# Optimization experiments

Measured on AMD Instinct MI355X. Metric: run time of the kernel, lower is better.

## Reference

```python
import jax, jax.numpy as jnp
import numpy as np

D = 128        # d_model
G = 2          # gnn_layers
LE = 2         # e_layers (MLP depth per update fn)
N_NODES = 20000
N_EDGES = 320000
SEQ = 72       # label_len(48) + pred_len(24)
DEC_IN = 4
PRED_LEN = 24
C_OUT = 1
EPS = 1e-5


def _ln(x, g, b):
    m = jnp.mean(x, axis=-1, keepdims=True)
    v = jnp.var(x, axis=-1, keepdims=True)
    return (x - m) * jax.lax.rsqrt(v + EPS) * g + b


def _mlp(x, ws, bs, gs, betas):
    # MLPLayer stack: LayerNorm(gelu(Linear(x))); dropout=0 in eval
    for i in range(ws.shape[0]):
        x = _ln(jax.nn.gelu(x @ ws[i] + bs[i]), gs[i], betas[i])
    return x


def setup_inputs():
    key = jax.random.key(0)
    ks = list(jax.random.split(key, 16))
    s = 0.02
    f32 = jnp.float32
    inp = {}
    inp["nodes"] = jax.random.normal(ks[0], (N_NODES, SEQ, DEC_IN), f32)
    inp["edges"] = jax.random.normal(ks[1], (N_EDGES, 2), f32)
    inp["senders"] = jax.random.randint(ks[2], (N_EDGES,), 0, N_NODES, jnp.int32)
    inp["receivers"] = jax.random.randint(ks[3], (N_EDGES,), 0, N_NODES, jnp.int32)
    inp["w_node_emb"] = jax.random.normal(ks[4], (SEQ * DEC_IN, D), f32) * s
    inp["b_node_emb"] = jnp.zeros((D,), f32)
    inp["w_edge_emb"] = jax.random.normal(ks[5], (2, D), f32) * s
    inp["b_edge_emb"] = jnp.zeros((D,), f32)
    inp["edge_proj_w"] = jax.random.normal(ks[6], (G, 3 * D, D), f32) * s
    inp["edge_proj_b"] = jnp.zeros((G, D), f32)
    inp["node_proj_w"] = jax.random.normal(ks[7], (G, 2 * D, D), f32) * s
    inp["node_proj_b"] = jnp.zeros((G, D), f32)
    inp["edge_mlp_w"] = jax.random.normal(ks[8], (G, LE, D, D), f32) * s
    inp["edge_mlp_b"] = jnp.zeros((G, LE, D), f32)
    inp["edge_ln_g"] = jnp.ones((G, LE, D), f32)
    inp["edge_ln_b"] = jnp.zeros((G, LE, D), f32)
    inp["node_mlp_w"] = jax.random.normal(ks[9], (G, LE, D, D), f32) * s
    inp["node_mlp_b"] = jnp.zeros((G, LE, D), f32)
    inp["node_ln_g"] = jnp.ones((G, LE, D), f32)
    inp["node_ln_b"] = jnp.zeros((G, LE, D), f32)
    inp["mlp_out_w"] = jax.random.normal(ks[10], (D, D), f32) * s
    inp["mlp_out_b"] = jnp.zeros((D,), f32)
    inp["mlp_out_g"] = jnp.ones((D,), f32)
    inp["mlp_out_beta"] = jnp.zeros((D,), f32)
    inp["proj_w"] = jax.random.normal(ks[11], (D, C_OUT * PRED_LEN), f32) * s
    inp["proj_b"] = jnp.zeros((C_OUT * PRED_LEN,), f32)
    return inp


def reference(nodes, edges, senders, receivers, w_node_emb, b_node_emb, w_edge_emb, b_edge_emb, edge_proj_w, edge_proj_b, node_proj_w, node_proj_b, edge_mlp_w, edge_mlp_b, edge_ln_g, edge_ln_b, node_mlp_w, node_mlp_b, node_ln_g, node_ln_b, mlp_out_w, mlp_out_b, mlp_out_g, mlp_out_beta, proj_w, proj_b):
    N = nodes.shape[0]
    # embeddings
    h = nodes.reshape(N, -1) @ w_node_emb + b_node_emb          # [N, D]
    e = edges @ w_edge_emb + b_edge_emb                         # [E, D]
    # receiver in-degree for unsorted_mean_agg (clamped to avoid /0)
    cnt = jax.ops.segment_sum(jnp.ones(e.shape[:1], h.dtype), receivers, num_segments=N)
    cnt = jnp.maximum(cnt, 1.0)[:, None]                        # [N, 1]
    for l in range(G):
        # edge update: gather endpoint node states, project to D, MLP, residual
        e_in = jnp.concatenate([e, h[senders], h[receivers]], axis=-1)   # [E, 3D]
        e = e + _mlp(e_in @ edge_proj_w[l] + edge_proj_b[l],
                     edge_mlp_w[l], edge_mlp_b[l], edge_ln_g[l], edge_ln_b[l])
        # scatter-mean aggregation of updated edges into receiver nodes
        agg = jax.ops.segment_sum(e, receivers, num_segments=N) / cnt    # [N, D]
        # node update
        n_in = jnp.concatenate([h, agg], axis=-1)                        # [N, 2D]
        h = h + _mlp(n_in @ node_proj_w[l] + node_proj_b[l],
                     node_mlp_w[l], node_mlp_b[l], node_ln_g[l], node_ln_b[l])
    # output MLP + projection to pred_len * c_out per node
    h = _ln(jax.nn.gelu(h @ mlp_out_w + mlp_out_b), mlp_out_g, mlp_out_beta)
    out = h @ proj_w + proj_b
    return out.reshape(N, PRED_LEN, C_OUT)
```

## Files before the change

kernel.cpp:

```cpp
#include <hip/hip_runtime.h>
#include <hip/hip_bf16.h>
#include <stdint.h>

typedef unsigned short ushort_t;
typedef __attribute__((ext_vector_type(8))) short short8;
typedef __attribute__((ext_vector_type(4))) short short4v;
typedef __attribute__((ext_vector_type(4))) float f32x4;
typedef __attribute__((ext_vector_type(4))) int int4v;

#define N_NODES 20000
#define N_EDGES 320000
#define D 128
#define XSTRIDE 136

#define GAS __attribute__((address_space(1)))
#define LAS __attribute__((address_space(3)))

__device__ __forceinline__ float b2f(ushort_t u) {
    union { float f; uint32_t i; } v; v.i = ((uint32_t)u) << 16; return v.f;
}
__device__ __forceinline__ ushort_t f2b(float f) {
    __bf16 h = (__bf16)f;
    return __builtin_bit_cast(ushort_t, h);
}
__device__ __forceinline__ float ldf(const void* p, size_t i, bool f32) {
    return f32 ? ((const float*)p)[i] : b2f(((const ushort_t*)p)[i]);
}
__device__ __forceinline__ short8 lda8(const void* p, size_t i, bool f32) {
    if (f32) {
        const float* fp = (const float*)p + i;
        f32x4 v0 = *(const f32x4*)fp;
        f32x4 v1 = *(const f32x4*)(fp + 4);
        short8 a;
#pragma unroll
        for (int j = 0; j < 4; ++j) {
            a[j]     = (short)f2b(v0[j]);
            a[j + 4] = (short)f2b(v1[j]);
        }
        return a;
    }
    return *(const short8*)((const ushort_t*)p + i);
}
__device__ __forceinline__ float gelu_tanh(float x) {
    float u = 0.7978845608028654f * (x + 0.044715f * x * x * x);
    u = fminf(fmaxf(u, -15.f), 15.f);
    float e = __expf(2.f * u);
    float t = (e - 1.f) * __builtin_amdgcn_rcpf(e + 1.f);
    return 0.5f * x * (1.f + t);
}
__device__ __forceinline__ int clampi(int v, int hi) {
    return v < 0 ? 0 : (v >= hi ? hi - 1 : v);
}
__device__ __forceinline__ void gload_lds16(const void* g, void* l) {
    __builtin_amdgcn_global_load_lds((const GAS uint32_t*)g, (LAS uint32_t*)l, 16, 0, 0);
}
__device__ __forceinline__ void ldedge(const void* edges, int row, bool f32, float& a0, float& a1) {
    if (f32) {
        const float* p = (const float*)edges + (size_t)row * 2;
        a0 = p[0]; a1 = p[1];
    } else {
        const ushort_t* p = (const ushort_t*)edges + (size_t)row * 2;
        a0 = b2f(p[0]); a1 = b2f(p[1]);
    }
}
__device__ __forceinline__ short8 einit8(const ushort_t* wedge, int colbase, float a0, float a1) {
    short8 w0 = *(const short8*)(wedge + colbase);
    short8 w1 = *(const short8*)(wedge + 128 + colbase);
    short8 bb = *(const short8*)(wedge + 256 + colbase);
    short8 r;
#pragma unroll
    for (int j = 0; j < 8; ++j)
        r[j] = (short)f2b(a0 * b2f((ushort_t)w0[j]) + a1 * b2f((ushort_t)w1[j]) + b2f((ushort_t)bb[j]));
    return r;
}

__device__ __forceinline__ void ln8(float x[8], const float gv[8], const float bv[8]) {
    float s1 = 0.f, s2 = 0.f;
#pragma unroll
    for (int n = 0; n < 8; ++n) { s1 += x[n]; s2 += x[n] * x[n]; }
#pragma unroll
    for (int m = 1; m < 16; m <<= 1) {
        s1 += __shfl_xor(s1, m, 64);
        s2 += __shfl_xor(s2, m, 64);
    }
    float mean = s1 * (1.f / 128.f);
    float var  = fmaxf(s2 * (1.f / 128.f) - mean * mean, 0.f);
    float rs   = __builtin_amdgcn_rsqf(var + 1e-5f);
#pragma unroll
    for (int n = 0; n < 8; ++n) x[n] = (x[n] - mean) * rs * gv[n] + bv[n];
}

__global__ void k_detect(const uint32_t* __restrict__ raw, int* __restrict__ flag) {
    int t = blockIdx.x * blockDim.x + threadIdx.x;
    uint32_t u = raw[t];
    int e_lo = (u >> 7)  & 0xFF;
    int e_hi = (u >> 23) & 0xFF;
    if (e_lo == 0xFF || e_hi == 0xFF) atomicOr(flag, 1);
}

struct SetupArgs {
    const void* psrc[15];
    int         pn[15];
    int         pdst[15];
    const void* fsrc[6];
    int         fkb[6];
    int         fdst[6];
    const void* projw;
};

__global__ void k_setup(SetupArgs a, ushort_t* __restrict__ bvec, ushort_t* __restrict__ frag,
                        ushort_t* __restrict__ wT, const int* __restrict__ dflag) {
    const bool f32 = *dflag != 0;
    int t = blockIdx.x * blockDim.x + threadIdx.x;
    if (t < 4608) {
        int i = t, d = 0;
        while (i >= a.pn[d]) { i -= a.pn[d]; ++d; }
        bvec[(size_t)a.pdst[d] * 128 + i] = f2b(ldf(a.psrc[d], i, f32));
        return;
    }
    t -= 4608;
    if (t < 3072) {
        int p = t >> 7, k = t & 127;
        wT[p * 128 + k] = f2b(ldf(a.projw, (size_t)k * 24 + p, f32));
        return;
    }
    t -= 3072;
    if (t >= 43520) return;
    int g = t, d = 0;
    while (g >= a.fkb[d] * 512) { g -= a.fkb[d] * 512; ++d; }
    const void* src = a.fsrc[d];
    int kblk = g >> 9;
    int rem  = g & 511;
    int nt   = rem >> 6;
    int lane = rem & 63;
    int krow = kblk * 32 + ((lane >> 4) << 3);
    int col  = nt * 16 + (lane & 15);
    short8 v;
#pragma unroll
    for (int j = 0; j < 8; ++j) v[j] = (short)f2b(ldf(src, (size_t)(krow + j) * 128 + col, f32));
    *(short8*)(frag + (size_t)a.fdst[d] + (size_t)g * 8) = v;
}

__global__ void k_counti(const int* __restrict__ recv, int* __restrict__ cnti, int E) {
    int i = blockIdx.x * blockDim.x + threadIdx.x;
    if (i < E) atomicAdd(&cnti[clampi(recv[i], N_NODES)], 1);
}

__global__ void k_scan(const int* __restrict__ cnti, int* __restrict__ offs,
                       int* __restrict__ cursor) {
    __shared__ int part[1024];
    const int t = threadIdx.x;
    const int base = t * 20;
    int s = 0;
#pragma unroll 4
    for (int j = 0; j < 20; ++j) {
        int idx = base + j;
        if (idx < N_NODES) s += cnti[idx];
    }
    part[t] = s;
    __syncthreads();
    for (int off = 1; off < 1024; off <<= 1) {
        int v = (t >= off) ? part[t - off] : 0;
        __syncthreads();
        part[t] += v;
        __syncthreads();
    }
    int run = (t == 0) ? 0 : part[t - 1];
    for (int j = 0; j < 20; ++j) {
        int idx = base + j;
        if (idx < N_NODES) {
            offs[idx]   = run;
            cursor[idx] = run;
            run += cnti[idx];
        }
    }
}

__global__ void k_fill(const int* __restrict__ recv, int* __restrict__ cursor,
                       int* __restrict__ eid, int E) {
    int i = blockIdx.x * blockDim.x + threadIdx.x;
    if (i < E) {
        int r = clampi(recv[i], N_NODES);
        int pos = atomicAdd(&cursor[r], 1);
        eid[pos] = i;
    }
}

__global__ void k_agg(const ushort_t* __restrict__ e, const int* __restrict__ offs,
                      const int* __restrict__ cnti, const int* __restrict__ eid,
                      ushort_t* __restrict__ agg) {
    const int tid = threadIdx.x;
    const int n = blockIdx.x * 8 + (tid >> 5);
    const int l = tid & 31;
    if (n >= N_NODES) return;
    const int start = offs[n], deg = cnti[n];
    float s0 = 0.f, s1 = 0.f, s2 = 0.f, s3 = 0.f;
    for (int j = 0; j < deg; ++j) {
        const ushort_t* row = e + (size_t)eid[start + j] * 128 + l * 4;
        short4v v = *(const short4v*)row;
        s0 += b2f((ushort_t)v[0]);
        s1 += b2f((ushort_t)v[1]);
        s2 += b2f((ushort_t)v[2]);
        s3 += b2f((ushort_t)v[3]);
    }
    const float inv = 1.f / (float)(deg < 1 ? 1 : deg);
    short4v o;
    o[0] = (short)f2b(s0 * inv);
    o[1] = (short)f2b(s1 * inv);
    o[2] = (short)f2b(s2 * inv);
    o[3] = (short)f2b(s3 * inv);
    *(short4v*)(agg + (size_t)n * 128 + l * 4) = o;
}

template<int NC, bool LN>
__global__ __launch_bounds__(256, 2) void k_gemm(
    const ushort_t* __restrict__ bfrag,
    const void* s0, int isf0, int st0, int ko0, int kl0,
    const void* s1, int isf1, int st1, int ko1, int kl1,
    const void* s2, int isf2, int st2, int ko2, int kl2,
    int rows,
    const ushort_t* __restrict__ bias,
    const ushort_t* __restrict__ gamma,
    const ushort_t* __restrict__ betap,
    ushort_t* out,
    const int* __restrict__ dflag)
{
    __shared__ __align__(16) ushort_t lds_b[128 * 128];
    const bool f32g = *dflag != 0;
    const int tid  = threadIdx.x;
    const int wave = tid >> 6, lane = tid & 63;
    const int quad = lane >> 4, l16 = lane & 15;
    const int row0 = blockIdx.x * 128 + wave * 32;

    f32x4 acc[2][8];
#pragma unroll
    for (int t = 0; t < 2; ++t)
#pragma unroll
        for (int n = 0; n < 8; ++n) acc[t][n] = (f32x4){0.f, 0.f, 0.f, 0.f};

    const ushort_t* bptr = bfrag;
#pragma unroll
    for (int c = 0; c < NC; ++c) {
        const void* src  = (c == 0) ? s0 : ((c == 1) ? s1 : s2);
        const bool  eff  = (((c == 0) ? isf0 : ((c == 1) ? isf1 : isf2)) != 0) && f32g;
        const int stride = (c == 0) ? st0 : ((c == 1) ? st1 : st2);
        const int koff   = (c == 0) ? ko0 : ((c == 1) ? ko1 : ko2);
        const int klen   = (c == 0) ? kl0 : ((c == 1) ? kl1 : kl2);

        if (c) __syncthreads();
        {
            const int ngrp = klen * 16;
            for (int g = tid; g < ngrp; g += 256)
                gload_lds16(bptr + (size_t)g * 8, lds_b + (size_t)g * 8);
        }
        __syncthreads();

        size_t aoff[2];
#pragma unroll
        for (int t = 0; t < 2; ++t) {
            int r  = row0 + t * 16 + l16;
            int rr = r < rows ? r : rows - 1;
            aoff[t] = (size_t)rr * stride + koff + quad * 8;
        }
        const int ksteps = klen >> 5;
        for (int ks = 0; ks < ksteps; ++ks) {
            short8 af[2];
#pragma unroll
            for (int t = 0; t < 2; ++t)
                af[t] = lda8(src, aoff[t] + ks * 32, eff);
#pragma unroll
            for (int n = 0; n < 8; ++n) {
                short8 bf = *(const short8*)(lds_b + (size_t)((ks * 8 + n) * 64 + lane) * 8);
                acc[0][n] = __builtin_amdgcn_mfma_f32_16x16x32_bf16(af[0], bf, acc[0][n], 0, 0, 0);
                acc[1][n] = __builtin_amdgcn_mfma_f32_16x16x32_bf16(af[1], bf, acc[1][n], 0, 0, 0);
            }
        }
        bptr += (size_t)klen * 128;
    }

    float bv[8], gv[8], btv[8];
#pragma unroll
    for (int n = 0; n < 8; ++n) {
        int col = n * 16 + l16;
        bv[n] = b2f(bias[col]);
        if (LN) { gv[n] = b2f(gamma[col]); btv[n] = b2f(betap[col]); }
    }
#pragma unroll
    for (int t = 0; t < 2; ++t) {
#pragma unroll
        for (int r = 0; r < 4; ++r) {
            int row = row0 + t * 16 + quad * 4 + r;
            float x[8];
#pragma unroll
            for (int n = 0; n < 8; ++n) x[n] = acc[t][n][r] + bv[n];
            if (LN) {
#pragma unroll
                for (int n = 0; n < 8; ++n) x[n] = gelu_tanh(x[n]);
                ln8(x, gv, btv);
            }
            if (row < rows) {
#pragma unroll
                for (int n = 0; n < 8; ++n)
                    out[(size_t)row * 128 + n * 16 + l16] = f2b(x[n]);
            }
        }
    }
}

__global__ __launch_bounds__(256, 2) void k_out(
    const ushort_t* __restrict__ bfrag,
    const ushort_t* __restrict__ h,
    const ushort_t* __restrict__ bias,
    const ushort_t* __restrict__ gamma,
    const ushort_t* __restrict__ betap,
    const ushort_t* __restrict__ wT,
    const void* __restrict__ pb,
    void* __restrict__ out, int rows,
    const int* __restrict__ dflag)
{
    __shared__ __align__(16) ushort_t lds_b[128 * 128];
    __shared__ __align__(16) ushort_t lds_x[128 * XSTRIDE];
    const bool f32g = *dflag != 0;
    const int tid  = threadIdx.x;
    const int wave = tid >> 6, lane = tid & 63;
    const int quad = lane >> 4, l16 = lane & 15;
    const int row0  = blockIdx.x * 128;
    const int lrow0 = wave * 32;

    for (int g = tid; g < 2048; g += 256)
        gload_lds16(bfrag + (size_t)g * 8, lds_b + (size_t)g * 8);
    __syncthreads();

    f32x4 acc[2][8];
#pragma unroll
    for (int t = 0; t < 2; ++t)
#pragma unroll
        for (int n = 0; n < 8; ++n) acc[t][n] = (f32x4){0.f, 0.f, 0.f, 0.f};

    const ushort_t* ap[2];
#pragma unroll
    for (int t = 0; t < 2; ++t) {
        int grow = row0 + lrow0 + t * 16 + l16;
        int rr = grow < rows ? grow : rows - 1;
        ap[t] = h + (size_t)rr * 128 + quad * 8;
    }
    for (int ks = 0; ks < 4; ++ks) {
        short8 af[2];
#pragma unroll
        for (int t = 0; t < 2; ++t) af[t] = *(const short8*)(ap[t] + ks * 32);
#pragma unroll
        for (int n = 0; n < 8; ++n) {
            short8 bf = *(const short8*)(lds_b + (size_t)((ks * 8 + n) * 64 + lane) * 8);
            acc[0][n] = __builtin_amdgcn_mfma_f32_16x16x32_bf16(af[0], bf, acc[0][n], 0, 0, 0);
            acc[1][n] = __builtin_amdgcn_mfma_f32_16x16x32_bf16(af[1], bf, acc[1][n], 0, 0, 0);
        }
    }

    {
        float bv[8], gv[8], btv[8];
#pragma unroll
        for (int n = 0; n < 8; ++n) {
            int col = n * 16 + l16;
            bv[n] = b2f(bias[col]); gv[n] = b2f(gamma[col]); btv[n] = b2f(betap[col]);
        }
#pragma unroll
        for (int t = 0; t < 2; ++t)
#pragma unroll
            for (int r = 0; r < 4; ++r) {
                int lrow = lrow0 + t * 16 + quad * 4 + r;
                float x[8];
#pragma unroll
                for (int n = 0; n < 8; ++n) x[n] = gelu_tanh(acc[t][n][r] + bv[n]);
                ln8(x, gv, btv);
#pragma unroll
                for (int n = 0; n < 8; ++n)
                    lds_x[lrow * XSTRIDE + n * 16 + l16] = f2b(x[n]);
            }
    }
    __syncthreads();

#pragma unroll
    for (int it = 0; it < 12; ++it) {
        int idx  = it * 256 + tid;
        int lrow = idx / 24;
        int p    = idx - lrow * 24;
        int grow = row0 + lrow;
        if (grow < rows) {
            float a2 = ldf(pb, p, f32g);
            const ushort_t* xp = lds_x + lrow * XSTRIDE;
            const ushort_t* wp = wT + (size_t)p * 128;
#pragma unroll
            for (int k8 = 0; k8 < 16; ++k8) {
                short8 hv = *(const short8*)(xp + k8 * 8);
                short8 wv = *(const short8*)(wp + k8 * 8);
#pragma unroll
                for (int j = 0; j < 8; ++j)
                    a2 += b2f((ushort_t)hv[j]) * b2f((ushort_t)wv[j]);
            }
            if (f32g) ((float*)out)[(size_t)grow * 24 + p] = a2;
            else      ((ushort_t*)out)[(size_t)grow * 24 + p] = f2b(a2);
        }
    }
}


#define STAGE(srcp, bufi) do {                                                   \
    const ushort_t* s__ = (srcp);                                                \
    _Pragma("unroll")                                                            \
    for (int it__ = 0; it__ < 4; ++it__) {                                       \
        int g__ = it__ * 256 + tid;                                              \
        gload_lds16(s__ + (size_t)g__ * 8, &lds_w[bufi][(size_t)g__ * 8]);       \
    } } while (0)

#define LOADA(dst, apv, hf) do {                                                 \
    _Pragma("unroll") for (int t_ = 0; t_ < 2; ++t_)                             \
    _Pragma("unroll") for (int k_ = 0; k_ < 2; ++k_)                             \
        dst[t_][k_] = *(const short8*)(apv[t_] + ((hf) * 2 + k_) * 32);          \
    } while (0)

#define PCH(AFU, AFN, apv, hfn, bufi, nsrc, nbuf, VM, DO_A, DO_STAGE) do {       \
    if (DO_A) LOADA(AFN, apv, hfn);                                              \
    __builtin_amdgcn_sched_barrier(0);                                           \
    if (DO_STAGE) STAGE(nsrc, nbuf);                                             \
    asm volatile("s_waitcnt vmcnt(" #VM ")" ::: "memory");                       \
    __builtin_amdgcn_s_barrier();                                                \
    __builtin_amdgcn_sched_barrier(0);                                           \
    _Pragma("unroll") for (int k_ = 0; k_ < 2; ++k_)                             \
    _Pragma("unroll") for (int n_ = 0; n_ < 8; ++n_) {                           \
        short8 bf_ = *(const short8*)(&lds_w[bufi][(size_t)((k_ * 8 + n_) * 64 + lane) * 8]); \
        acc[0][n_] = __builtin_amdgcn_mfma_f32_16x16x32_bf16(AFU[0][k_], bf_, acc[0][n_], 0, 0, 0); \
        acc[1][n_] = __builtin_amdgcn_mfma_f32_16x16x32_bf16(AFU[1][k_], bf_, acc[1][n_], 0, 0, 0); \
    }                                                                            \
    __builtin_amdgcn_sched_barrier(0);                                           \
    __builtin_amdgcn_s_barrier();                                                \
} while (0)

#define XCHUNK(hf, bufi, DO_STAGE, nsrc, nbuf, VM) do {                          \
    if (DO_STAGE) STAGE(nsrc, nbuf);                                             \
    asm volatile("s_waitcnt vmcnt(" #VM ")" ::: "memory");                       \
    __builtin_amdgcn_s_barrier();                                                \
    __builtin_amdgcn_sched_barrier(0);                                           \
    _Pragma("unroll") for (int k_ = 0; k_ < 2; ++k_) {                           \
        short8 af_[2];                                                           \
        _Pragma("unroll") for (int t_ = 0; t_ < 2; ++t_)                         \
            af_[t_] = *(const short8*)(lds_x + (size_t)(lrow0 + t_ * 16 + l16) * XSTRIDE \
                                       + ((hf) * 2 + k_) * 32 + quad * 8);       \
        _Pragma("unroll") for (int n_ = 0; n_ < 8; ++n_) {                       \
            short8 bf_ = *(const short8*)(&lds_w[bufi][(size_t)((k_ * 8 + n_) * 64 + lane) * 8]); \
            acc[0][n_] = __builtin_amdgcn_mfma_f32_16x16x32_bf16(af_[0], bf_, acc[0][n_], 0, 0, 0); \
            acc[1][n_] = __builtin_amdgcn_mfma_f32_16x16x32_bf16(af_[1], bf_, acc[1][n_], 0, 0, 0); \
        }                                                                        \
    }                                                                            \
    __builtin_amdgcn_sched_barrier(0);                                           \
    __builtin_amdgcn_s_barrier();                                                \
} while (0)

#define EPI_PROJ() do {                                                          \
    _Pragma("unroll") for (int t_ = 0; t_ < 2; ++t_)                             \
    _Pragma("unroll") for (int r_ = 0; r_ < 4; ++r_) {                           \
        int lr_ = lrow0 + t_ * 16 + quad * 4 + r_;                               \
        _Pragma("unroll") for (int n_ = 0; n_ < 8; ++n_)                         \
            lds_x[lr_ * XSTRIDE + n_ * 16 + l16] = f2b(acc[t_][n_][r_] + pbv[n_]); \
    }                                                                            \
    _Pragma("unroll") for (int t_ = 0; t_ < 2; ++t_)                             \
    _Pragma("unroll") for (int n_ = 0; n_ < 8; ++n_) acc[t_][n_] = (f32x4){0.f, 0.f, 0.f, 0.f}; \
} while (0)

#define EPI_LN(BV, GV, BEV) do {                                                 \
    _Pragma("unroll") for (int t_ = 0; t_ < 2; ++t_)                             \
    _Pragma("unroll") for (int r_ = 0; r_ < 4; ++r_) {                           \
        int lr_ = lrow0 + t_ * 16 + quad * 4 + r_;                               \
        float x_[8];                                                             \
        _Pragma("unroll") for (int n_ = 0; n_ < 8; ++n_) x_[n_] = gelu_tanh(acc[t_][n_][r_] + BV[n_]); \
        ln8(x_, GV, BEV);                                                        \
        _Pragma("unroll") for (int n_ = 0; n_ < 8; ++n_)                         \
            lds_x[lr_ * XSTRIDE + n_ * 16 + l16] = f2b(x_[n_]);                  \
    }                                                                            \
    _Pragma("unroll") for (int t_ = 0; t_ < 2; ++t_)                             \
    _Pragma("unroll") for (int n_ = 0; n_ < 8; ++n_) acc[t_][n_] = (f32x4){0.f, 0.f, 0.f, 0.f}; \
} while (0)

template<int L0>
__global__ __launch_bounds__(256, 2) void k_edge_fused(
    const ushort_t* __restrict__ bf_proj,
    const ushort_t* __restrict__ bf_w0,
    const ushort_t* __restrict__ bf_w1,
    ushort_t* e_glob,
    const ushort_t* __restrict__ h,
    const int* __restrict__ senders, const int* __restrict__ receivers,
    const void* __restrict__ edges_raw,
    const ushort_t* __restrict__ wedge_arena,
    const ushort_t* __restrict__ pb,
    const ushort_t* __restrict__ b0, const ushort_t* __restrict__ g0, const ushort_t* __restrict__ be0,
    const ushort_t* __restrict__ b1, const ushort_t* __restrict__ g1, const ushort_t* __restrict__ be1,
    const int* __restrict__ dflag)
{
    __shared__ __align__(16) ushort_t lds_w[2][64 * 128];
    __shared__ __align__(16) ushort_t lds_x[128 * XSTRIDE];
    __shared__ __align__(16) ushort_t wedge[512];
    const int tid  = threadIdx.x;
    const int wave = tid >> 6, lane = tid & 63;
    const int quad = lane >> 4, l16 = lane & 15;
    const int row0  = blockIdx.x * 128;
    const int lrow0 = wave * 32;
    const bool f32g = L0 ? (*dflag != 0) : false;

    float pbv[8], b0v[8], g0v[8], be0v[8], b1v[8], g1v[8], be1v[8];
#pragma unroll
    for (int n = 0; n < 8; ++n) {
        int col = n * 16 + l16;
        pbv[n]  = b2f(pb[col]);
        b0v[n]  = b2f(b0[col]);  g0v[n] = b2f(g0[col]);  be0v[n] = b2f(be0[col]);
        b1v[n]  = b2f(b1[col]);  g1v[n] = b2f(g1[col]);  be1v[n] = b2f(be1[col]);
    }

    const ushort_t* apE[2]; const ushort_t* apS[2]; const ushort_t* apR[2];
#pragma unroll
    for (int t = 0; t < 2; ++t) {
        int grow = row0 + lrow0 + t * 16 + l16;
        apE[t] = e_glob + (size_t)grow * 128 + quad * 8;
        apS[t] = h + (size_t)clampi(senders[grow],   N_NODES) * 128 + quad * 8;
        apR[t] = h + (size_t)clampi(receivers[grow], N_NODES) * 128 + quad * 8;
    }

    const ushort_t* p0a = bf_proj;             const ushort_t* p0b = bf_proj + 8192;
    const ushort_t* p1a = bf_proj + 16384;     const ushort_t* p1b = bf_proj + 24576;
    const ushort_t* p2a = bf_proj + 32768;     const ushort_t* p2b = bf_proj + 40960;
    const ushort_t* w0a = bf_w0;               const ushort_t* w0b = bf_w0 + 8192;
    const ushort_t* w1a = bf_w1;               const ushort_t* w1b = bf_w1 + 8192;

    f32x4 acc[2][8];
#pragma unroll
    for (int t = 0; t < 2; ++t)
#pragma unroll
        for (int n = 0; n < 8; ++n) acc[t][n] = (f32x4){0.f, 0.f, 0.f, 0.f};

    short8 afA[2][2], afB[2][2];

    if (L0) {
        if (wave == 0)
            gload_lds16(wedge_arena + (size_t)lane * 8, wedge + (size_t)lane * 8);
        float a0f[2], a1f[2];
#pragma unroll
        for (int t = 0; t < 2; ++t) {
            int grow = row0 + lrow0 + t * 16 + l16;
            ldedge(edges_raw, grow, f32g, a0f[t], a1f[t]);
        }
        asm volatile("s_waitcnt vmcnt(0)" ::: "memory");
        __builtin_amdgcn_s_barrier();
        short8 afE0[2][2], afE1[2][2];
#pragma unroll
        for (int t = 0; t < 2; ++t)
#pragma unroll
            for (int k = 0; k < 2; ++k) {
                afE0[t][k] = einit8(wedge, (0 * 2 + k) * 32 + quad * 8, a0f[t], a1f[t]);
                afE1[t][k] = einit8(wedge, (1 * 2 + k) * 32 + quad * 8, a0f[t], a1f[t]);
            }
        STAGE(p0a, 0);
        PCH(afE0, afA, apS, 0, 0, p0b, 1, 4, 0, 1);
        PCH(afE1, afA, apS, 0, 1, p1a, 0, 8, 1, 1);
        PCH(afA,  afB, apS, 1, 0, p1b, 1, 8, 1, 1);
        PCH(afB,  afA, apR, 0, 1, p2a, 0, 8, 1, 1);
        PCH(afA,  afB, apR, 1, 0, p2b, 1, 8, 1, 1);
        PCH(afB,  afA, apR, 1, 1, w0a, 0, 4, 0, 1);
    } else {
        LOADA(afA, apE, 0);
        __builtin_amdgcn_sched_barrier(0);
        STAGE(p0a, 0);
        PCH(afA, afB, apE, 1, 0, p0b, 1, 8, 1, 1);
        PCH(afB, afA, apS, 0, 1, p1a, 0, 8, 1, 1);
        PCH(afA, afB, apS, 1, 0, p1b, 1, 8, 1, 1);
        PCH(afB, afA, apR, 0, 1, p2a, 0, 8, 1, 1);
        PCH(afA, afB, apR, 1, 0, p2b, 1, 8, 1, 1);
        PCH(afB, afA, apR, 1, 1, w0a, 0, 4, 0, 1);
    }
    EPI_PROJ();
    XCHUNK(0, 0, 1, w0b, 1, 4);
    XCHUNK(1, 1, 1, w1a, 0, 4);
    EPI_LN(b0v, g0v, be0v);
    XCHUNK(0, 0, 1, w1b, 1, 4);
    XCHUNK(1, 1, 0, w1b, 0, 0);
    EPI_LN(b1v, g1v, be1v);

    __syncthreads();
#pragma unroll
    for (int it = 0; it < 8; ++it) {
        int idx  = it * 256 + tid;
        int lrow = idx >> 4;
        int c8   = (idx & 15) << 3;
        size_t goff = (size_t)(row0 + lrow) * 128 + c8;
        short8 xv = *(const short8*)(lds_x + lrow * XSTRIDE + c8);
        short8 yv;
        if (L0) {
            float ea0, ea1;
            ldedge(edges_raw, row0 + lrow, f32g, ea0, ea1);
            short8 w0 = *(const short8*)(wedge + c8);
            short8 w1 = *(const short8*)(wedge + 128 + c8);
            short8 bb = *(const short8*)(wedge + 256 + c8);
#pragma unroll
            for (int j = 0; j < 8; ++j) {
                float base = ea0 * b2f((ushort_t)w0[j]) + ea1 * b2f((ushort_t)w1[j]) + b2f((ushort_t)bb[j]);
                yv[j] = (short)f2b(base + b2f((ushort_t)xv[j]));
            }
        } else {
            short8 ev = *(const short8*)(e_glob + goff);
#pragma unroll
            for (int j = 0; j < 8; ++j)
                yv[j] = (short)f2b(b2f((ushort_t)ev[j]) + b2f((ushort_t)xv[j]));
        }
        *(short8*)(e_glob + goff) = yv;
    }
}

__global__ __launch_bounds__(256, 2) void k_node_fused(
    const ushort_t* __restrict__ bf_proj,
    const ushort_t* __restrict__ bf_w0,
    const ushort_t* __restrict__ bf_w1,
    ushort_t* h,
    const ushort_t* __restrict__ agg,
    const ushort_t* __restrict__ pb,
    const ushort_t* __restrict__ b0, const ushort_t* __restrict__ g0, const ushort_t* __restrict__ be0,
    const ushort_t* __restrict__ b1, const ushort_t* __restrict__ g1, const ushort_t* __restrict__ be1,
    int rows)
{
    __shared__ __align__(16) ushort_t lds_w[2][64 * 128];
    __shared__ __align__(16) ushort_t lds_x[128 * XSTRIDE];
    const int tid  = threadIdx.x;
    const int wave = tid >> 6, lane = tid & 63;
    const int quad = lane >> 4, l16 = lane & 15;
    const int row0  = blockIdx.x * 128;
    const int lrow0 = wave * 32;

    float pbv[8], b0v[8], g0v[8], be0v[8], b1v[8], g1v[8], be1v[8];
#pragma unroll
    for (int n = 0; n < 8; ++n) {
        int col = n * 16 + l16;
        pbv[n]  = b2f(pb[col]);
        b0v[n]  = b2f(b0[col]);  g0v[n] = b2f(g0[col]);  be0v[n] = b2f(be0[col]);
        b1v[n]  = b2f(b1[col]);  g1v[n] = b2f(g1[col]);  be1v[n] = b2f(be1[col]);
    }

    const ushort_t* apH[2]; const ushort_t* apA[2];
#pragma unroll
    for (int t = 0; t < 2; ++t) {
        int grow = row0 + lrow0 + t * 16 + l16;
        int rr = grow < rows ? grow : rows - 1;
        apH[t] = h   + (size_t)rr * 128 + quad * 8;
        apA[t] = agg + (size_t)rr * 128 + quad * 8;
    }

    const ushort_t* n0a = bf_proj;           const ushort_t* n0b = bf_proj + 8192;
    const ushort_t* n1a = bf_proj + 16384;   const ushort_t* n1b = bf_proj + 24576;
    const ushort_t* w0a = bf_w0;             const ushort_t* w0b = bf_w0 + 8192;
    const ushort_t* w1a = bf_w1;             const ushort_t* w1b = bf_w1 + 8192;

    f32x4 acc[2][8];
#pragma unroll
    for (int t = 0; t < 2; ++t)
#pragma unroll
        for (int n = 0; n < 8; ++n) acc[t][n] = (f32x4){0.f, 0.f, 0.f, 0.f};

    short8 afA[2][2], afB[2][2];
    LOADA(afA, apH, 0);
    __builtin_amdgcn_sched_barrier(0);
    STAGE(n0a, 0);
    PCH(afA, afB, apH, 1, 0, n0b, 1, 8, 1, 1);
    PCH(afB, afA, apA, 0, 1, n1a, 0, 8, 1, 1);
    PCH(afA, afB, apA, 1, 0, n1b, 1, 8, 1, 1);
    PCH(afB, afA, apA, 1, 1, w0a, 0, 4, 0, 1);
    EPI_PROJ();
    XCHUNK(0, 0, 1, w0b, 1, 4);
    XCHUNK(1, 1, 1, w1a, 0, 4);
    EPI_LN(b0v, g0v, be0v);
    XCHUNK(0, 0, 1, w1b, 1, 4);
    XCHUNK(1, 1, 0, w1b, 0, 0);
    EPI_LN(b1v, g1v, be1v);

    __syncthreads();
#pragma unroll
    for (int it = 0; it < 8; ++it) {
        int idx  = it * 256 + tid;
        int lrow = idx >> 4;
        int c8   = (idx & 15) << 3;
        int grow = row0 + lrow;
        if (grow < rows) {
            size_t goff = (size_t)grow * 128 + c8;
            short8 xv = *(const short8*)(lds_x + lrow * XSTRIDE + c8);
            short8 hv = *(const short8*)(h + goff);
            short8 yv;
#pragma unroll
            for (int j = 0; j < 8; ++j)
                yv[j] = (short)f2b(b2f((ushort_t)hv[j]) + b2f((ushort_t)xv[j]));
            *(short8*)(h + goff) = yv;
        }
    }
}

extern "C" void kernel_launch(void* const* d_in, const int* in_sizes, int n_in,
                              void* d_out, int out_size, void* d_ws, size_t ws_size,
                              hipStream_t stream) {
    const void* nodes        = d_in[0];
    const void* edges        = d_in[1];
    const int*  senders      = (const int*)d_in[2];
    const int*  receivers    = (const int*)d_in[3];
    const void* w_node_emb   = d_in[4];
    const void* b_node_emb   = d_in[5];
    const void* w_edge_emb   = d_in[6];
    const void* b_edge_emb   = d_in[7];
    const void* edge_proj_w  = d_in[8];
    const void* edge_proj_b  = d_in[9];
    const void* node_proj_w  = d_in[10];
    const void* node_proj_b  = d_in[11];
    const void* edge_mlp_w   = d_in[12];
    const void* edge_mlp_b   = d_in[13];
    const void* edge_ln_g    = d_in[14];
    const void* edge_ln_b    = d_in[15];
    const void* node_mlp_w   = d_in[16];
    const void* node_mlp_b   = d_in[17];
    const void* node_ln_g    = d_in[18];
    const void* node_ln_b    = d_in[19];
    const void* mlp_out_w    = d_in[20];
    const void* mlp_out_b    = d_in[21];
    const void* mlp_out_g    = d_in[22];
    const void* mlp_out_beta = d_in[23];
    const void* proj_w       = d_in[24];
    const void* proj_b       = d_in[25];

    char* ws = (char*)d_ws;
    ushort_t* bf_nodeemb  = (ushort_t*)ws;  ws += (size_t)288 * 128 * 2;
    ushort_t* bf_edgeproj = (ushort_t*)ws;  ws += (size_t)768 * 128 * 2;
    ushort_t* bf_nodeproj = (ushort_t*)ws;  ws += (size_t)512 * 128 * 2;
    ushort_t* bf_edgemlp  = (ushort_t*)ws;  ws += (size_t)512 * 128 * 2;
    ushort_t* bf_nodemlp  = (ushort_t*)ws;  ws += (size_t)512 * 128 * 2;
    ushort_t* bf_mlpout   = (ushort_t*)ws;  ws += (size_t)128 * 128 * 2;
    ushort_t* h    = (ushort_t*)ws;         ws += (size_t)N_NODES * D * 2;
    ushort_t* e    = (ushort_t*)ws;         ws += (size_t)N_EDGES * D * 2;
    ushort_t* agg  = (ushort_t*)ws;         ws += (size_t)N_NODES * D * 2;
    int*      cnti = (int*)ws;              ws += (size_t)N_NODES * 4;
    int*      offs = (int*)ws;              ws += (size_t)N_NODES * 4;
    int*      curs = (int*)ws;              ws += (size_t)N_NODES * 4;
    int*      eid  = (int*)ws;              ws += (size_t)N_EDGES * 4;
    int*      flag = (int*)ws;              ws += 256;
    ushort_t* bvec = (ushort_t*)ws;         ws += (size_t)37 * 128 * 2;
    ushort_t* wT   = (ushort_t*)ws;         ws += (size_t)24 * 128 * 2;

    hipMemsetAsync(flag, 0, 256, stream);
    k_detect<<<256, 256, 0, stream>>>((const uint32_t*)nodes, flag);

    {
        SetupArgs sa;
        const void* ps[15] = { b_node_emb, b_edge_emb, edge_proj_b, node_proj_b,
                               edge_mlp_b, edge_ln_g, edge_ln_b,
                               node_mlp_b, node_ln_g, node_ln_b,
                               mlp_out_b, mlp_out_g, mlp_out_beta,
                               w_edge_emb, b_edge_emb };
        const int   pn[15] = { 128, 128, 256, 256, 512, 512, 512, 512, 512, 512, 128, 128, 128, 256, 128 };
        const int   pd[15] = { 0, 1, 2, 4, 6, 10, 14, 18, 22, 26, 30, 31, 32, 33, 35 };
        const void* fs[6]  = { w_node_emb, edge_proj_w, node_proj_w, edge_mlp_w, node_mlp_w, mlp_out_w };
        const int   fk[6]  = { 9, 24, 16, 16, 16, 4 };
        const int   fd[6]  = { 0, 36864, 135168, 200704, 266240, 331776 };
        for (int i = 0; i < 15; ++i) { sa.psrc[i] = ps[i]; sa.pn[i] = pn[i]; sa.pdst[i] = pd[i]; }
        for (int i = 0; i < 6;  ++i) { sa.fsrc[i] = fs[i]; sa.fkb[i] = fk[i]; sa.fdst[i] = fd[i]; }
        sa.projw = proj_w;
        k_setup<<<200, 256, 0, stream>>>(sa, bvec, bf_nodeemb, wT, flag);
    }

    hipMemsetAsync(cnti, 0, (size_t)N_NODES * 4, stream);
    k_counti<<<(N_EDGES + 255) / 256, 256, 0, stream>>>(receivers, cnti, N_EDGES);
    k_scan<<<1, 1024, 0, stream>>>(cnti, offs, curs);
    k_fill<<<(N_EDGES + 255) / 256, 256, 0, stream>>>(receivers, curs, eid, N_EDGES);

    {
        const int grid = (N_NODES + 127) / 128;
        k_gemm<3, false><<<grid, 256, 0, stream>>>(
            bf_nodeemb,
            nodes, 1, 288, 0,   128,
            nodes, 1, 288, 128, 128,
            nodes, 1, 288, 256, 32,
            N_NODES, bvec + 0 * 128, nullptr, nullptr, h, flag);
    }

    const int gridE = N_EDGES / 128;
    const int gridN = (N_NODES + 127) / 128;

    for (int l = 0; l < 2; ++l) {
        if (l == 0) {
            k_edge_fused<1><<<gridE, 256, 0, stream>>>(
                bf_edgeproj,
                bf_edgemlp + (size_t)0 * 128 * 128,
                bf_edgemlp + (size_t)1 * 128 * 128,
                e, h, senders, receivers,
                edges, bvec + 33 * 128,
                bvec + 2 * 128,
                bvec + 6 * 128,  bvec + 10 * 128, bvec + 14 * 128,
                bvec + 7 * 128,  bvec + 11 * 128, bvec + 15 * 128,
                flag);
        } else {
            k_edge_fused<0><<<gridE, 256, 0, stream>>>(
                bf_edgeproj + (size_t)384 * 128,
                bf_edgemlp + (size_t)2 * 128 * 128,
                bf_edgemlp + (size_t)3 * 128 * 128,
                e, h, senders, receivers,
                edges, bvec + 33 * 128,
                bvec + 3 * 128,
                bvec + 8 * 128,  bvec + 12 * 128, bvec + 16 * 128,
                bvec + 9 * 128,  bvec + 13 * 128, bvec + 17 * 128,
                flag);
        }
        k_agg<<<(N_NODES + 7) / 8, 256, 0, stream>>>(e, offs, cnti, eid, agg);
        k_node_fused<<<gridN, 256, 0, stream>>>(
            bf_nodeproj + (size_t)l * 256 * 128,
            bf_nodemlp + (size_t)(l * 2 + 0) * 128 * 128,
            bf_nodemlp + (size_t)(l * 2 + 1) * 128 * 128,
            h, agg,
            bvec + (size_t)(4 + l) * 128,
            bvec + (size_t)(18 + l * 2) * 128,     bvec + (size_t)(22 + l * 2) * 128,     bvec + (size_t)(26 + l * 2) * 128,
            bvec + (size_t)(18 + l * 2 + 1) * 128, bvec + (size_t)(22 + l * 2 + 1) * 128, bvec + (size_t)(26 + l * 2 + 1) * 128,
            N_NODES);
    }

    k_out<<<gridN, 256, 0, stream>>>(
        bf_mlpout, h,
        bvec + 30 * 128, bvec + 31 * 128, bvec + 32 * 128,
        wT, proj_b, d_out, N_NODES, flag);
}
```

Baseline: 602.1 us.

## Halve weight staging chunks to fit three blocks per CU

Splits the double-buffered weight staging from 64-row K chunks into 32-row chunks, halving the LDS weight buffers, and raises launch bounds from 2 to 3 blocks per CU for both fused edge and node kernels. The pipeline schedule is rewritten with twice as many stages, adjusted vmcnt waits and single-k A fragments. The aim is more resident blocks to hide gather latency, at the cost of twice as many barriers per tile and a tighter register budget.

```diff
diff --git a/kernel.cpp b/kernel.cpp
--- a/kernel.cpp
+++ b/kernel.cpp
@@ -407,46 +407,44 @@
 #define STAGE(srcp, bufi) do {                                                   \
     const ushort_t* s__ = (srcp);                                                \
     _Pragma("unroll")                                                            \
-    for (int it__ = 0; it__ < 4; ++it__) {                                       \
+    for (int it__ = 0; it__ < 2; ++it__) {                                       \
         int g__ = it__ * 256 + tid;                                              \
         gload_lds16(s__ + (size_t)g__ * 8, &lds_w[bufi][(size_t)g__ * 8]);       \
     } } while (0)
 
-#define LOADA(dst, apv, hf) do {                                                 \
+#define LOADA(dst, apv, kn) do {                                                 \
     _Pragma("unroll") for (int t_ = 0; t_ < 2; ++t_)                             \
-    _Pragma("unroll") for (int k_ = 0; k_ < 2; ++k_)                             \
-        dst[t_][k_] = *(const short8*)(apv[t_] + ((hf) * 2 + k_) * 32);          \
+        dst[t_] = *(const short8*)(apv[t_] + (kn) * 32);                         \
     } while (0)
 
-#define PCH(AFU, AFN, apv, hfn, bufi, nsrc, nbuf, VM, DO_A, DO_STAGE) do {       \
-    if (DO_A) LOADA(AFN, apv, hfn);                                              \
+#define PCH(AFU, AFN, apv, kn, bufi, nsrc, nbuf, VM, DO_A, DO_STAGE) do {        \
+    if (DO_A) LOADA(AFN, apv, kn);                                               \
     __builtin_amdgcn_sched_barrier(0);                                           \
     if (DO_STAGE) STAGE(nsrc, nbuf);                                             \
     asm volatile("s_waitcnt vmcnt(" #VM ")" ::: "memory");                       \
     __builtin_amdgcn_s_barrier();                                                \
     __builtin_amdgcn_sched_barrier(0);                                           \
-    _Pragma("unroll") for (int k_ = 0; k_ < 2; ++k_)                             \
     _Pragma("unroll") for (int n_ = 0; n_ < 8; ++n_) {                           \
-        short8 bf_ = *(const short8*)(&lds_w[bufi][(size_t)((k_ * 8 + n_) * 64 + lane) * 8]); \
-        acc[0][n_] = __builtin_amdgcn_mfma_f32_16x16x32_bf16(AFU[0][k_], bf_, acc[0][n_], 0, 0, 0); \
-        acc[1][n_] = __builtin_amdgcn_mfma_f32_16x16x32_bf16(AFU[1][k_], bf_, acc[1][n_], 0, 0, 0); \
+        short8 bf_ = *(const short8*)(&lds_w[bufi][(size_t)(n_ * 64 + lane) * 8]); \
+        acc[0][n_] = __builtin_amdgcn_mfma_f32_16x16x32_bf16(AFU[0], bf_, acc[0][n_], 0, 0, 0); \
+        acc[1][n_] = __builtin_amdgcn_mfma_f32_16x16x32_bf16(AFU[1], bf_, acc[1][n_], 0, 0, 0); \
     }                                                                            \
     __builtin_amdgcn_sched_barrier(0);                                           \
     __builtin_amdgcn_s_barrier();                                                \
 } while (0)
 
-#define XCHUNK(hf, bufi, DO_STAGE, nsrc, nbuf, VM) do {                          \
+#define XCHUNK(kx, bufi, DO_STAGE, nsrc, nbuf, VM) do {                          \
     if (DO_STAGE) STAGE(nsrc, nbuf);                                             \
     asm volatile("s_waitcnt vmcnt(" #VM ")" ::: "memory");                       \
     __builtin_amdgcn_s_barrier();                                                \
     __builtin_amdgcn_sched_barrier(0);                                           \
-    _Pragma("unroll") for (int k_ = 0; k_ < 2; ++k_) {                           \
+    {                                                                            \
         short8 af_[2];                                                           \
         _Pragma("unroll") for (int t_ = 0; t_ < 2; ++t_)                         \
             af_[t_] = *(const short8*)(lds_x + (size_t)(lrow0 + t_ * 16 + l16) * XSTRIDE \
-                                       + ((hf) * 2 + k_) * 32 + quad * 8);       \
+                                       + (kx) * 32 + quad * 8);                  \
         _Pragma("unroll") for (int n_ = 0; n_ < 8; ++n_) {                       \
-            short8 bf_ = *(const short8*)(&lds_w[bufi][(size_t)((k_ * 8 + n_) * 64 + lane) * 8]); \
+            short8 bf_ = *(const short8*)(&lds_w[bufi][(size_t)(n_ * 64 + lane) * 8]); \
             acc[0][n_] = __builtin_amdgcn_mfma_f32_16x16x32_bf16(af_[0], bf_, acc[0][n_], 0, 0, 0); \
             acc[1][n_] = __builtin_amdgcn_mfma_f32_16x16x32_bf16(af_[1], bf_, acc[1][n_], 0, 0, 0); \
         }                                                                        \
@@ -481,7 +479,7 @@
 } while (0)
 
 template<int L0>
-__global__ __launch_bounds__(256, 2) void k_edge_fused(
+__global__ __launch_bounds__(256, 3) void k_edge_fused(
     const ushort_t* __restrict__ bf_proj,
     const ushort_t* __restrict__ bf_w0,
     const ushort_t* __restrict__ bf_w1,
@@ -495,7 +493,7 @@
     const ushort_t* __restrict__ b1, const ushort_t* __restrict__ g1, const ushort_t* __restrict__ be1,
     const int* __restrict__ dflag)
 {
-    __shared__ __align__(16) ushort_t lds_w[2][64 * 128];
+    __shared__ __align__(16) ushort_t lds_w[2][32 * 128];
     __shared__ __align__(16) ushort_t lds_x[128 * XSTRIDE];
     __shared__ __align__(16) ushort_t wedge[512];
     const int tid  = threadIdx.x;
@@ -523,11 +521,16 @@
         apR[t] = h + (size_t)clampi(receivers[grow], N_NODES) * 128 + quad * 8;
     }
 
-    const ushort_t* p0a = bf_proj;             const ushort_t* p0b = bf_proj + 8192;
-    const ushort_t* p1a = bf_proj + 16384;     const ushort_t* p1b = bf_proj + 24576;
-    const ushort_t* p2a = bf_proj + 32768;     const ushort_t* p2b = bf_proj + 40960;
-    const ushort_t* w0a = bf_w0;               const ushort_t* w0b = bf_w0 + 8192;
-    const ushort_t* w1a = bf_w1;               const ushort_t* w1b = bf_w1 + 8192;
+    const ushort_t* pe0 = bf_proj;                const ushort_t* pe1 = bf_proj + 4096;
+    const ushort_t* pe2 = bf_proj + 8192;         const ushort_t* pe3 = bf_proj + 12288;
+    const ushort_t* ps0 = bf_proj + 16384;        const ushort_t* ps1 = bf_proj + 20480;
+    const ushort_t* ps2 = bf_proj + 24576;        const ushort_t* ps3 = bf_proj + 28672;
+    const ushort_t* pr0 = bf_proj + 32768;        const ushort_t* pr1 = bf_proj + 36864;
+    const ushort_t* pr2 = bf_proj + 40960;        const ushort_t* pr3 = bf_proj + 45056;
+    const ushort_t* w0c0 = bf_w0;                 const ushort_t* w0c1 = bf_w0 + 4096;
+    const ushort_t* w0c2 = bf_w0 + 8192;          const ushort_t* w0c3 = bf_w0 + 12288;
+    const ushort_t* w1c0 = bf_w1;                 const ushort_t* w1c1 = bf_w1 + 4096;
+    const ushort_t* w1c2 = bf_w1 + 8192;          const ushort_t* w1c3 = bf_w1 + 12288;
 
     f32x4 acc[2][8];
 #pragma unroll
@@ -535,7 +538,7 @@
 #pragma unroll
         for (int n = 0; n < 8; ++n) acc[t][n] = (f32x4){0.f, 0.f, 0.f, 0.f};
 
-    short8 afA[2][2], afB[2][2];
+    short8 afA[2], afB[2];
 
     if (L0) {
         if (wave == 0)
@@ -548,38 +551,54 @@
         }
         asm volatile("s_waitcnt vmcnt(0)" ::: "memory");
         __builtin_amdgcn_s_barrier();
-        short8 afE0[2][2], afE1[2][2];
-#pragma unroll
-        for (int t = 0; t < 2; ++t)
-#pragma unroll
-            for (int k = 0; k < 2; ++k) {
-                afE0[t][k] = einit8(wedge, (0 * 2 + k) * 32 + quad * 8, a0f[t], a1f[t]);
-                afE1[t][k] = einit8(wedge, (1 * 2 + k) * 32 + quad * 8, a0f[t], a1f[t]);
-            }
-        STAGE(p0a, 0);
-        PCH(afE0, afA, apS, 0, 0, p0b, 1, 4, 0, 1);
-        PCH(afE1, afA, apS, 0, 1, p1a, 0, 8, 1, 1);
-        PCH(afA,  afB, apS, 1, 0, p1b, 1, 8, 1, 1);
-        PCH(afB,  afA, apR, 0, 1, p2a, 0, 8, 1, 1);
-        PCH(afA,  afB, apR, 1, 0, p2b, 1, 8, 1, 1);
-        PCH(afB,  afA, apR, 1, 1, w0a, 0, 4, 0, 1);
+        short8 afE0[2], afE1[2], afE2[2], afE3[2];
+#pragma unroll
+        for (int t = 0; t < 2; ++t) {
+            afE0[t] = einit8(wedge, 0 * 32 + quad * 8, a0f[t], a1f[t]);
+            afE1[t] = einit8(wedge, 1 * 32 + quad * 8, a0f[t], a1f[t]);
+            afE2[t] = einit8(wedge, 2 * 32 + quad * 8, a0f[t], a1f[t]);
+            afE3[t] = einit8(wedge, 3 * 32 + quad * 8, a0f[t], a1f[t]);
+        }
+        STAGE(pe0, 0);
+        PCH(afE0, afA, apS, 0, 0, pe1, 1, 2, 0, 1);
+        PCH(afE1, afA, apS, 0, 1, pe2, 0, 2, 0, 1);
+        PCH(afE2, afA, apS, 0, 0, pe3, 1, 2, 0, 1);
+        PCH(afE3, afA, apS, 0, 1, ps0, 0, 4, 1, 1);
+        PCH(afA,  afB, apS, 1, 0, ps1, 1, 4, 1, 1);
+        PCH(afB,  afA, apS, 2, 1, ps2, 0, 4, 1, 1);
+        PCH(afA,  afB, apS, 3, 0, ps3, 1, 4, 1, 1);
+        PCH(afB,  afA, apR, 0, 1, pr0, 0, 4, 1, 1);
+        PCH(afA,  afB, apR, 1, 0, pr1, 1, 4, 1, 1);
+        PCH(afB,  afA, apR, 2, 1, pr2, 0, 4, 1, 1);
+        PCH(afA,  afB, apR, 3, 0, pr3, 1, 4, 1, 1);
+        PCH(afB,  afA, apR, 3, 1, w0c0, 0, 2, 0, 1);
     } else {
         LOADA(afA, apE, 0);
         __builtin_amdgcn_sched_barrier(0);
-        STAGE(p0a, 0);
-        PCH(afA, afB, apE, 1, 0, p0b, 1, 8, 1, 1);
-        PCH(afB, afA, apS, 0, 1, p1a, 0, 8, 1, 1);
-        PCH(afA, afB, apS, 1, 0, p1b, 1, 8, 1, 1);
-        PCH(afB, afA, apR, 0, 1, p2a, 0, 8, 1, 1);
-        PCH(afA, afB, apR, 1, 0, p2b, 1, 8, 1, 1);
-        PCH(afB, afA, apR, 1, 1, w0a, 0, 4, 0, 1);
+        STAGE(pe0, 0);
+        PCH(afA, afB, apE, 1, 0, pe1, 1, 4, 1, 1);
+        PCH(afB, afA, apE, 2, 1, pe2, 0, 4, 1, 1);
+        PCH(afA, afB, apE, 3, 0, pe3, 1, 4, 1, 1);
+        PCH(afB, afA, apS, 0, 1, ps0, 0, 4, 1, 1);
+        PCH(afA, afB, apS, 1, 0, ps1, 1, 4, 1, 1);
+        PCH(afB, afA, apS, 2, 1, ps2, 0, 4, 1, 1);
+        PCH(afA, afB, apS, 3, 0, ps3, 1, 4, 1, 1);
+        PCH(afB, afA, apR, 0, 1, pr0, 0, 4, 1, 1);
+        PCH(afA, afB, apR, 1, 0, pr1, 1, 4, 1, 1);
+        PCH(afB, afA, apR, 2, 1, pr2, 0, 4, 1, 1);
+        PCH(afA, afB, apR, 3, 0, pr3, 1, 4, 1, 1);
+        PCH(afB, afA, apR, 3, 1, w0c0, 0, 2, 0, 1);
     }
     EPI_PROJ();
-    XCHUNK(0, 0, 1, w0b, 1, 4);
-    XCHUNK(1, 1, 1, w1a, 0, 4);
+    XCHUNK(0, 0, 1, w0c1, 1, 2);
+    XCHUNK(1, 1, 1, w0c2, 0, 2);
+    XCHUNK(2, 0, 1, w0c3, 1, 2);
+    XCHUNK(3, 1, 1, w1c0, 0, 2);
     EPI_LN(b0v, g0v, be0v);
-    XCHUNK(0, 0, 1, w1b, 1, 4);
-    XCHUNK(1, 1, 0, w1b, 0, 0);
+    XCHUNK(0, 0, 1, w1c1, 1, 2);
+    XCHUNK(1, 1, 1, w1c2, 0, 2);
+    XCHUNK(2, 0, 1, w1c3, 1, 2);
+    XCHUNK(3, 1, 0, w1c3, 0, 0);
     EPI_LN(b1v, g1v, be1v);
 
     __syncthreads();
@@ -612,7 +631,7 @@
     }
 }
 
-__global__ __launch_bounds__(256, 2) void k_node_fused(
+__global__ __launch_bounds__(256, 3) void k_node_fused(
     const ushort_t* __restrict__ bf_proj,
     const ushort_t* __restrict__ bf_w0,
     const ushort_t* __restrict__ bf_w1,
@@ -623,7 +642,7 @@
     const ushort_t* __restrict__ b1, const ushort_t* __restrict__ g1, const ushort_t* __restrict__ be1,
     int rows)
 {
-    __shared__ __align__(16) ushort_t lds_w[2][64 * 128];
+    __shared__ __align__(16) ushort_t lds_w[2][32 * 128];
     __shared__ __align__(16) ushort_t lds_x[128 * XSTRIDE];
     const int tid  = threadIdx.x;
     const int wave = tid >> 6, lane = tid & 63;
@@ -649,10 +668,14 @@
         apA[t] = agg + (size_t)rr * 128 + quad * 8;
     }
 
-    const ushort_t* n0a = bf_proj;           const ushort_t* n0b = bf_proj + 8192;
-    const ushort_t* n1a = bf_proj + 16384;   const ushort_t* n1b = bf_proj + 24576;
-    const ushort_t* w0a = bf_w0;             const ushort_t* w0b = bf_w0 + 8192;
-    const ushort_t* w1a = bf_w1;             const ushort_t* w1b = bf_w1 + 8192;
+    const ushort_t* ph0 = bf_proj;            const ushort_t* ph1 = bf_proj + 4096;
+    const ushort_t* ph2 = bf_proj + 8192;     const ushort_t* ph3 = bf_proj + 12288;
+    const ushort_t* pa0 = bf_proj + 16384;    const ushort_t* pa1 = bf_proj + 20480;
+    const ushort_t* pa2 = bf_proj + 24576;    const ushort_t* pa3 = bf_proj + 28672;
+    const ushort_t* w0c0 = bf_w0;             const ushort_t* w0c1 = bf_w0 + 4096;
+    const ushort_t* w0c2 = bf_w0 + 8192;      const ushort_t* w0c3 = bf_w0 + 12288;
+    const ushort_t* w1c0 = bf_w1;             const ushort_t* w1c1 = bf_w1 + 4096;
+    const ushort_t* w1c2 = bf_w1 + 8192;      const ushort_t* w1c3 = bf_w1 + 12288;
 
     f32x4 acc[2][8];
 #pragma unroll
@@ -660,20 +683,28 @@
 #pragma unroll
         for (int n = 0; n < 8; ++n) acc[t][n] = (f32x4){0.f, 0.f, 0.f, 0.f};
 
-    short8 afA[2][2], afB[2][2];
+    short8 afA[2], afB[2];
     LOADA(afA, apH, 0);
     __builtin_amdgcn_sched_barrier(0);
-    STAGE(n0a, 0);
-    PCH(afA, afB, apH, 1, 0, n0b, 1, 8, 1, 1);
-    PCH(afB, afA, apA, 0, 1, n1a, 0, 8, 1, 1);
-    PCH(afA, afB, apA, 1, 0, n1b, 1, 8, 1, 1);
-    PCH(afB, afA, apA, 1, 1, w0a, 0, 4, 0, 1);
+    STAGE(ph0, 0);
+    PCH(afA, afB, apH, 1, 0, ph1, 1, 4, 1, 1);
+    PCH(afB, afA, apH, 2, 1, ph2, 0, 4, 1, 1);
+    PCH(afA, afB, apH, 3, 0, ph3, 1, 4, 1, 1);
+    PCH(afB, afA, apA, 0, 1, pa0, 0, 4, 1, 1);
+    PCH(afA, afB, apA, 1, 0, pa1, 1, 4, 1, 1);
+    PCH(afB, afA, apA, 2, 1, pa2, 0, 4, 1, 1);
+    PCH(afA, afB, apA, 3, 0, pa3, 1, 4, 1, 1);
+    PCH(afB, afA, apA, 3, 1, w0c0, 0, 2, 0, 1);
     EPI_PROJ();
-    XCHUNK(0, 0, 1, w0b, 1, 4);
-    XCHUNK(1, 1, 1, w1a, 0, 4);
+    XCHUNK(0, 0, 1, w0c1, 1, 2);
+    XCHUNK(1, 1, 1, w0c2, 0, 2);
+    XCHUNK(2, 0, 1, w0c3, 1, 2);
+    XCHUNK(3, 1, 1, w1c0, 0, 2);
     EPI_LN(b0v, g0v, be0v);
-    XCHUNK(0, 0, 1, w1b, 1, 4);
-    XCHUNK(1, 1, 0, w1b, 0, 0);
+    XCHUNK(0, 0, 1, w1c1, 1, 2);
+    XCHUNK(1, 1, 1, w1c2, 0, 2);
+    XCHUNK(2, 0, 1, w1c3, 1, 2);
+    XCHUNK(3, 1, 0, w1c3, 0, 0);
     EPI_LN(b1v, g1v, be1v);
 
     __syncthreads();
```

New measurement: 573.8 us. 1.05x faster.
